# Kernel tuning notes

Measured on AMD Instinct MI355X. Metric: run time of the kernel, lower is better.

The kernel has to match this reference:

```python
import jax, jax.numpy as jnp
import numpy as np

B, S, D = 4, 2048, 768
H = 12
HD = D // H  # 64


def setup_inputs() -> dict:
    key = jax.random.key(0)
    k1, k2, k3 = jax.random.split(key, 3)
    scale_qkv = (6.0 / (D + 3 * D)) ** 0.5  # xavier_uniform bound
    scale_o = (6.0 / (D + D)) ** 0.5
    return {
        "x": jax.random.normal(k1, (B, S, D), dtype=jnp.float32),
        "w_qkv": jax.random.uniform(k2, (3 * D, D), dtype=jnp.float32, minval=-scale_qkv, maxval=scale_qkv),
        "b_qkv": jnp.zeros((3 * D,), dtype=jnp.float32),
        "w_o": jax.random.uniform(k3, (D, D), dtype=jnp.float32, minval=-scale_o, maxval=scale_o),
        "b_o": jnp.zeros((D,), dtype=jnp.float32),
    }


def reference(x, w_qkv, b_qkv, w_o, b_o):
    b, s, _ = x.shape
    # qkv projection: [B,S,3D]
    qkv = jnp.einsum("bsd,ed->bse", x, w_qkv) + b_qkv
    # [B,S,H,3*HD] -> [B,H,S,3*HD]
    qkv = qkv.reshape(b, s, H, 3 * HD).transpose(0, 2, 1, 3)
    q, k, v = jnp.split(qkv, 3, axis=-1)  # each [B,H,S,HD]
    # scaled dot-product attention (full score matrix, as in source)
    attn_logits = jnp.einsum("bhqd,bhkd->bhqk", q, k) / np.sqrt(HD).astype(np.float32)
    attention = jax.nn.softmax(attn_logits, axis=-1)
    values = jnp.einsum("bhqk,bhkd->bhqd", attention, v)
    # merge heads: [B,S,D]
    values = values.transpose(0, 2, 1, 3).reshape(b, s, D)
    out = jnp.einsum("bsd,ed->bse", values, w_o) + b_o
    return out
```

## Files before the change

kernel.cpp:

```cpp
#include <hip/hip_runtime.h>
#include <hip/hip_bf16.h>

#define BB 4
#define SS 2048
#define DD 768
#define HH 12
#define HDD 64
#define QKVW 2304

typedef _Float16 h8 __attribute__((ext_vector_type(8)));
typedef _Float16 h2 __attribute__((ext_vector_type(2)));
typedef __fp16 fp16x2 __attribute__((ext_vector_type(2)));
typedef float f4 __attribute__((ext_vector_type(4)));
typedef unsigned int u4 __attribute__((ext_vector_type(4)));

struct __align__(8) Half4 { _Float16 x, y, z, w; };
struct __align__(8) H2x2 { h2 a, b; };

#define QSCALE 0.18033688011112042f

__device__ __forceinline__ h2 pk_cvt(float a, float b) {
    fp16x2 r = __builtin_amdgcn_cvt_pkrtz(a, b);
    return __builtin_bit_cast(h2, r);
}

__device__ __forceinline__ float fexp2(float x) {
    return __builtin_amdgcn_exp2f(x);
}

__device__ __forceinline__ void pl_swap32(unsigned &a, unsigned &b) {
    asm("v_permlane32_swap_b32 %0, %1" : "+v"(a), "+v"(b));
}
__device__ __forceinline__ void pl_swap16(unsigned &a, unsigned &b) {
    asm("v_permlane16_swap_b32 %0, %1" : "+v"(a), "+v"(b));
}

#define N4_X   (BB * SS * DD / 4)
#define N4_WQ  (QKVW * DD / 4)
#define N4_WO  (DD * DD / 4)
#define N4_ALL (N4_X + N4_WQ + N4_WO)

__global__ __launch_bounds__(256) void cvt_all(const float* __restrict__ x,
                                               const float* __restrict__ wq,
                                               const float* __restrict__ wo,
                                               _Float16* __restrict__ xh,
                                               _Float16* __restrict__ wqh,
                                               _Float16* __restrict__ woh) {
    int i = blockIdx.x * 256 + threadIdx.x;
    const float* src;
    _Float16* dst;
    if (i < N4_X) {
        src = x; dst = xh;
    } else if (i < N4_X + N4_WQ) {
        i -= N4_X; src = wq; dst = wqh;
    } else {
        i -= N4_X + N4_WQ; src = wo; dst = woh;
    }
    const float4 v = ((const float4*)src)[i];
    Half4 h = {(_Float16)v.x, (_Float16)v.y, (_Float16)v.z, (_Float16)v.w};
    ((Half4*)dst)[i] = h;
}

__device__ __forceinline__ void gload16(const _Float16* g, _Float16* l) {
    __builtin_amdgcn_global_load_lds(
        (const __attribute__((address_space(1))) unsigned int*)g,
        (__attribute__((address_space(3))) unsigned int*)l, 16, 0, 0);
}

template <int EPI>
__global__ __launch_bounds__(256) void gemm_f16(const _Float16* __restrict__ A,
                                                const _Float16* __restrict__ B,
                                                const float* __restrict__ bias,
                                                float* __restrict__ Cf,
                                                _Float16* __restrict__ Ch,
                                                _Float16* __restrict__ VTg,
                                                int M, int N, int K) {
    __shared__ alignas(16) _Float16 Ash[128 * 64];
    __shared__ alignas(16) _Float16 Bsh[128 * 64];

    const int tid = threadIdx.x;
    const int lane = tid & 63;
    const int w = tid >> 6;
    const int l15 = lane & 15;
    const int qd = lane >> 4;
    const int wm = w & 1;
    const int wn = w >> 1;
    const int m0 = blockIdx.y * 128;
    const int n0 = blockIdx.x * 128;
    const int ldsb = w * 512;

    f4 acc[4][4];
#pragma unroll
    for (int mt = 0; mt < 4; ++mt)
#pragma unroll
        for (int nt = 0; nt < 4; ++nt) acc[mt][nt] = (f4){0.f, 0.f, 0.f, 0.f};

    const _Float16* Ab = A + (size_t)m0 * K;
    const _Float16* Bb = B + (size_t)n0 * K;

    const int srow = tid >> 3;
    const int cg = ((tid & 7) ^ (srow & 7)) * 8;
    const int x7 = l15 & 7;

    for (int k0 = 0; k0 < K; k0 += 64) {
        __syncthreads();
#pragma unroll
        for (int i = 0; i < 4; ++i) {
            const size_t gsrc = (size_t)(i * 32 + srow) * K + k0 + cg;
            gload16(Ab + gsrc, Ash + i * 2048 + ldsb);
            gload16(Bb + gsrc, Bsh + i * 2048 + ldsb);
        }
        __syncthreads();

#pragma unroll
        for (int s = 0; s < 2; ++s) {
            h8 aF[4], bF[4];
#pragma unroll
            for (int mt = 0; mt < 4; ++mt)
                aF[mt] = *(const h8*)&Ash[(wm * 64 + mt * 16 + l15) * 64
                                          + (((s * 4 + qd) ^ x7) << 3)];
#pragma unroll
            for (int nt = 0; nt < 4; ++nt)
                bF[nt] = *(const h8*)&Bsh[(wn * 64 + nt * 16 + l15) * 64
                                          + (((s * 4 + qd) ^ x7) << 3)];
#pragma unroll
            for (int mt = 0; mt < 4; ++mt)
#pragma unroll
                for (int nt = 0; nt < 4; ++nt)
                    acc[mt][nt] = __builtin_amdgcn_mfma_f32_16x16x32_f16(
                        bF[nt], aF[mt], acc[mt][nt], 0, 0, 0);
        }
    }

#pragma unroll
    for (int mt = 0; mt < 4; ++mt) {
        const int m = m0 + wm * 64 + mt * 16 + l15;
#pragma unroll
        for (int nt = 0; nt < 4; ++nt) {
            const int nb = n0 + wn * 64 + nt * 16 + qd * 4;
            const float4 bv = *(const float4*)(bias + nb);
            f4 v = acc[mt][nt];
            v[0] += bv.x; v[1] += bv.y; v[2] += bv.z; v[3] += bv.w;
            if (EPI == 0) {
                *(float4*)(Cf + (size_t)m * N + nb) = (float4){v[0], v[1], v[2], v[3]};
            } else {
                const int typ = (nb >> 6) % 3;
                if (typ == 2) {
                    const int h_ = nb / 192;
                    const int d0 = nb - h_ * 192 - 128;
                    _Float16* vtp = VTg + ((size_t)(m >> 11) * 768 + h_ * 64 + d0) * 2048
                                    + (m & 2047);
                    vtp[0] = (_Float16)v[0];
                    vtp[2048] = (_Float16)v[1];
                    vtp[2 * 2048] = (_Float16)v[2];
                    vtp[3 * 2048] = (_Float16)v[3];
                } else {
                    if (typ == 0) {
                        v[0] *= QSCALE; v[1] *= QSCALE; v[2] *= QSCALE; v[3] *= QSCALE;
                    }
                    H2x2 pk;
                    pk.a = pk_cvt(v[0], v[1]);
                    pk.b = pk_cvt(v[2], v[3]);
                    *(H2x2*)(Ch + (size_t)m * N + nb) = pk;
                }
            }
        }
    }
}

__global__ __launch_bounds__(256, 3) void attn_mfma(const _Float16* __restrict__ qkvh,
                                                    const _Float16* __restrict__ vT,
                                                    _Float16* __restrict__ vh) {
    __shared__ alignas(16) _Float16 Kh[2][64 * 64];
    __shared__ alignas(16) _Float16 VTs[2][64 * 64];

    const int tid = threadIdx.x;
    const int lane = tid & 63;
    const int w = tid >> 6;
    const int l15 = lane & 15;
    const int qd = lane >> 4;
    const int h = blockIdx.y;
    const int b = blockIdx.z;
    const int qbase = blockIdx.x * 128 + w * 32;

    const size_t bhrow = (size_t)b * SS;
    const int hcol = h * 192;
    const int x7 = l15 & 7;

    h8 bQ[2][2];
#pragma unroll
    for (int nt = 0; nt < 2; ++nt)
#pragma unroll
        for (int kc = 0; kc < 2; ++kc)
            bQ[nt][kc] = *(const h8*)(qkvh + (bhrow + qbase + nt * 16 + l15) * QKVW
                                      + hcol + kc * 32 + qd * 8);

    f4 O[4][2];
#pragma unroll
    for (int dt = 0; dt < 4; ++dt)
#pragma unroll
        for (int nt = 0; nt < 2; ++nt) O[dt][nt] = (f4){0.f, 0.f, 0.f, 0.f};
    f4 lacc[2] = {(f4){0.f, 0.f, 0.f, 0.f}, (f4){0.f, 0.f, 0.f, 0.f}};

    h8 ones;
#pragma unroll
    for (int i = 0; i < 8; ++i) ones[i] = (_Float16)1.0f;

    const int srow = tid >> 3;
    const int cgx = ((tid & 7) ^ (srow & 7)) << 3;
    const _Float16* kgbase = qkvh + bhrow * QKVW + hcol + 64 + cgx;
    const _Float16* vgbase = vT + ((size_t)b * 768 + h * 64) * 2048 + cgx;
    const int ldso = w * 512;

    auto stage = [&](int kt, int buf) {
#pragma unroll
        for (int i = 0; i < 2; ++i) {
            gload16(kgbase + (size_t)(kt * 64 + i * 32 + srow) * QKVW,
                    &Kh[buf][i * 2048 + ldso]);
            gload16(vgbase + (size_t)(i * 32 + srow) * 2048 + kt * 64,
                    &VTs[buf][i * 2048 + ldso]);
        }
    };

    stage(0, 0);

    for (int kt = 0; kt < SS / 64; ++kt) {
        const int buf = kt & 1;
        __syncthreads();
        if (kt + 1 < SS / 64) stage(kt + 1, buf ^ 1);

        h8 aK[4][2];
#pragma unroll
        for (int mt = 0; mt < 4; ++mt)
#pragma unroll
            for (int kc = 0; kc < 2; ++kc)
                aK[mt][kc] = *(const h8*)&Kh[buf][(mt * 16 + l15) * 64
                                                  + (((kc * 4 + qd) ^ x7) << 3)];
        h8 aV[4][2];
#pragma unroll
        for (int dt = 0; dt < 4; ++dt)
#pragma unroll
            for (int kc = 0; kc < 2; ++kc)
                aV[dt][kc] = *(const h8*)&VTs[buf][(dt * 16 + l15) * 64
                                                   + (((kc * 4 + qd) ^ x7) << 3)];

        h8 bP[2][2];
#pragma unroll
        for (int nt = 0; nt < 2; ++nt) {
            unsigned c[4][2];
            __builtin_amdgcn_s_setprio(1);
#pragma unroll
            for (int mt = 0; mt < 4; ++mt) {
                f4 z = (f4){0.f, 0.f, 0.f, 0.f};
                z = __builtin_amdgcn_mfma_f32_16x16x32_f16(aK[mt][0], bQ[nt][0], z, 0, 0, 0);
                z = __builtin_amdgcn_mfma_f32_16x16x32_f16(aK[mt][1], bQ[nt][1], z, 0, 0, 0);
                c[mt][0] = __builtin_bit_cast(unsigned, pk_cvt(fexp2(z[0]), fexp2(z[1])));
                c[mt][1] = __builtin_bit_cast(unsigned, pk_cvt(fexp2(z[2]), fexp2(z[3])));
            }
            __builtin_amdgcn_s_setprio(0);
#pragma unroll
            for (int kc = 0; kc < 2; ++kc) {
                unsigned x0 = c[2 * kc][0], y0 = c[2 * kc + 1][0];
                pl_swap32(x0, y0);
                pl_swap16(x0, y0);
                unsigned x1 = c[2 * kc][1], y1 = c[2 * kc + 1][1];
                pl_swap32(x1, y1);
                pl_swap16(x1, y1);
                u4 t = (u4){x0, x1, y0, y1};
                bP[nt][kc] = __builtin_bit_cast(h8, t);
            }
        }

        __builtin_amdgcn_s_setprio(1);
#pragma unroll
        for (int nt = 0; nt < 2; ++nt) {
            lacc[nt] = __builtin_amdgcn_mfma_f32_16x16x32_f16(ones, bP[nt][0], lacc[nt], 0, 0, 0);
            lacc[nt] = __builtin_amdgcn_mfma_f32_16x16x32_f16(ones, bP[nt][1], lacc[nt], 0, 0, 0);
        }
#pragma unroll
        for (int dt = 0; dt < 4; ++dt)
#pragma unroll
            for (int nt = 0; nt < 2; ++nt) {
                O[dt][nt] = __builtin_amdgcn_mfma_f32_16x16x32_f16(aV[dt][0], bP[nt][0], O[dt][nt], 0, 0, 0);
                O[dt][nt] = __builtin_amdgcn_mfma_f32_16x16x32_f16(aV[dt][1], bP[nt][1], O[dt][nt], 0, 0, 0);
            }
        __builtin_amdgcn_s_setprio(0);
    }

#pragma unroll
    for (int nt = 0; nt < 2; ++nt) {
        const float linv = 1.0f / lacc[nt][0];
        const size_t row = bhrow + qbase + nt * 16 + l15;
#pragma unroll
        for (int dt = 0; dt < 4; ++dt) {
            f4 o = O[dt][nt];
            Half4 oh;
            oh.x = (_Float16)(o[0] * linv);
            oh.y = (_Float16)(o[1] * linv);
            oh.z = (_Float16)(o[2] * linv);
            oh.w = (_Float16)(o[3] * linv);
            *(Half4*)(vh + row * DD + h * 64 + dt * 16 + qd * 4) = oh;
        }
    }
}

extern "C" void kernel_launch(void* const* d_in, const int* in_sizes, int n_in,
                              void* d_out, int out_size, void* d_ws, size_t ws_size,
                              hipStream_t stream) {
    const float* x     = (const float*)d_in[0];
    const float* w_qkv = (const float*)d_in[1];
    const float* b_qkv = (const float*)d_in[2];
    const float* w_o   = (const float*)d_in[3];
    const float* b_o   = (const float*)d_in[4];
    float* out = (float*)d_out;

    const int M = BB * SS;

    _Float16* p = (_Float16*)d_ws;
    _Float16* qkv_h = p;  p += (size_t)M * QKVW;
    _Float16* vT = p;     p += (size_t)BB * DD * SS;
    _Float16* xh = p;     p += (size_t)M * DD;
    _Float16* vh = p;     p += (size_t)M * DD;
    _Float16* wqh = p;    p += (size_t)QKVW * DD;
    _Float16* woh = p;    p += (size_t)DD * DD;

    cvt_all<<<N4_ALL / 256, 256, 0, stream>>>(x, w_qkv, w_o, xh, wqh, woh);

    gemm_f16<1><<<dim3(QKVW / 128, M / 128), 256, 0, stream>>>(
        xh, wqh, b_qkv, nullptr, qkv_h, vT, M, QKVW, DD);

    attn_mfma<<<dim3(SS / 128, HH, BB), 256, 0, stream>>>(qkv_h, vT, vh);

    gemm_f16<0><<<dim3(DD / 128, M / 128), 256, 0, stream>>>(
        vh, woh, b_o, out, nullptr, nullptr, M, DD, DD);
}
```

Baseline: 221.6 us.

## Split attention key tiles across two wave groups with LDS reduction

Doubles the attention block to 512 threads so each 64-key tile is split between two wave groups, each handling 32 keys for the same 32 query rows. Partial O accumulators and row sums are combined through shared memory at the end before normalization. This halves per-wave MFMA and LDS work per tile, aiming at more latency hiding and wave-level parallelism. The cost is extra redundant Q loads and exp work per wave, plus an epilogue with several barriers and LDS traffic. Softmax has no max subtraction, so a plain sum of partials is correct.

```diff
diff --git a/kernel.cpp b/kernel.cpp
--- a/kernel.cpp
+++ b/kernel.cpp
@@ -168,7 +168,7 @@
     }
 }
 
-__global__ __launch_bounds__(256, 3) void attn_mfma(const _Float16* __restrict__ qkvh,
+__global__ __launch_bounds__(512, 6) void attn_mfma(const _Float16* __restrict__ qkvh,
                                                     const _Float16* __restrict__ vT,
                                                     _Float16* __restrict__ vh) {
     __shared__ alignas(16) _Float16 Kh[2][64 * 64];
@@ -177,11 +177,13 @@
     const int tid = threadIdx.x;
     const int lane = tid & 63;
     const int w = tid >> 6;
+    const int qg = w & 3;
+    const int kh = w >> 2;
     const int l15 = lane & 15;
     const int qd = lane >> 4;
     const int h = blockIdx.y;
     const int b = blockIdx.z;
-    const int qbase = blockIdx.x * 128 + w * 32;
+    const int qbase = blockIdx.x * 128 + qg * 32;
 
     const size_t bhrow = (size_t)b * SS;
     const int hcol = h * 192;
@@ -206,20 +208,15 @@
 #pragma unroll
     for (int i = 0; i < 8; ++i) ones[i] = (_Float16)1.0f;
 
-    const int srow = tid >> 3;
-    const int cgx = ((tid & 7) ^ (srow & 7)) << 3;
-    const _Float16* kgbase = qkvh + bhrow * QKVW + hcol + 64 + cgx;
-    const _Float16* vgbase = vT + ((size_t)b * 768 + h * 64) * 2048 + cgx;
+    const int trow = (tid >> 3) & 63;
+    const int cgx = ((tid & 7) ^ (trow & 7)) << 3;
+    const _Float16* kgbase = qkvh + (bhrow + trow) * QKVW + hcol + 64 + cgx;
+    const _Float16* vgbase = vT + ((size_t)b * 768 + h * 64 + trow) * 2048 + cgx;
     const int ldso = w * 512;
 
     auto stage = [&](int kt, int buf) {
-#pragma unroll
-        for (int i = 0; i < 2; ++i) {
-            gload16(kgbase + (size_t)(kt * 64 + i * 32 + srow) * QKVW,
-                    &Kh[buf][i * 2048 + ldso]);
-            gload16(vgbase + (size_t)(i * 32 + srow) * 2048 + kt * 64,
-                    &VTs[buf][i * 2048 + ldso]);
-        }
+        gload16(kgbase + (size_t)kt * 64 * QKVW, &Kh[buf][ldso]);
+        gload16(vgbase + kt * 64, &VTs[buf][ldso]);
     };
 
     stage(0, 0);
@@ -229,28 +226,26 @@
         __syncthreads();
         if (kt + 1 < SS / 64) stage(kt + 1, buf ^ 1);
 
-        h8 aK[4][2];
-#pragma unroll
-        for (int mt = 0; mt < 4; ++mt)
+        h8 aK[2][2];
+#pragma unroll
+        for (int mt = 0; mt < 2; ++mt)
 #pragma unroll
             for (int kc = 0; kc < 2; ++kc)
-                aK[mt][kc] = *(const h8*)&Kh[buf][(mt * 16 + l15) * 64
+                aK[mt][kc] = *(const h8*)&Kh[buf][(kh * 32 + mt * 16 + l15) * 64
                                                   + (((kc * 4 + qd) ^ x7) << 3)];
-        h8 aV[4][2];
+        h8 aV[4];
 #pragma unroll
         for (int dt = 0; dt < 4; ++dt)
-#pragma unroll
-            for (int kc = 0; kc < 2; ++kc)
-                aV[dt][kc] = *(const h8*)&VTs[buf][(dt * 16 + l15) * 64
-                                                   + (((kc * 4 + qd) ^ x7) << 3)];
-
-        h8 bP[2][2];
+            aV[dt] = *(const h8*)&VTs[buf][(dt * 16 + l15) * 64
+                                           + (((kh * 4 + qd) ^ x7) << 3)];
+
+        h8 bP[2];
 #pragma unroll
         for (int nt = 0; nt < 2; ++nt) {
-            unsigned c[4][2];
+            unsigned c[2][2];
             __builtin_amdgcn_s_setprio(1);
 #pragma unroll
-            for (int mt = 0; mt < 4; ++mt) {
+            for (int mt = 0; mt < 2; ++mt) {
                 f4 z = (f4){0.f, 0.f, 0.f, 0.f};
                 z = __builtin_amdgcn_mfma_f32_16x16x32_f16(aK[mt][0], bQ[nt][0], z, 0, 0, 0);
                 z = __builtin_amdgcn_mfma_f32_16x16x32_f16(aK[mt][1], bQ[nt][1], z, 0, 0, 0);
@@ -258,48 +253,77 @@
                 c[mt][1] = __builtin_bit_cast(unsigned, pk_cvt(fexp2(z[2]), fexp2(z[3])));
             }
             __builtin_amdgcn_s_setprio(0);
-#pragma unroll
-            for (int kc = 0; kc < 2; ++kc) {
-                unsigned x0 = c[2 * kc][0], y0 = c[2 * kc + 1][0];
-                pl_swap32(x0, y0);
-                pl_swap16(x0, y0);
-                unsigned x1 = c[2 * kc][1], y1 = c[2 * kc + 1][1];
-                pl_swap32(x1, y1);
-                pl_swap16(x1, y1);
-                u4 t = (u4){x0, x1, y0, y1};
-                bP[nt][kc] = __builtin_bit_cast(h8, t);
+            unsigned x0 = c[0][0], y0 = c[1][0];
+            pl_swap32(x0, y0);
+            pl_swap16(x0, y0);
+            unsigned x1 = c[0][1], y1 = c[1][1];
+            pl_swap32(x1, y1);
+            pl_swap16(x1, y1);
+            u4 t = (u4){x0, x1, y0, y1};
+            bP[nt] = __builtin_bit_cast(h8, t);
+        }
+
+        __builtin_amdgcn_s_setprio(1);
+#pragma unroll
+        for (int nt = 0; nt < 2; ++nt)
+            lacc[nt] = __builtin_amdgcn_mfma_f32_16x16x32_f16(ones, bP[nt], lacc[nt], 0, 0, 0);
+#pragma unroll
+        for (int dt = 0; dt < 4; ++dt)
+#pragma unroll
+            for (int nt = 0; nt < 2; ++nt)
+                O[dt][nt] = __builtin_amdgcn_mfma_f32_16x16x32_f16(aV[dt], bP[nt], O[dt][nt], 0, 0, 0);
+        __builtin_amdgcn_s_setprio(0);
+    }
+
+    __syncthreads();
+    f4* cmb = (f4*)&Kh[0][0];
+    float* lcmb = (float*)&VTs[0][0];
+    const int ps = (qg * 64 + lane) * 4;
+
+    if (kh == 1) {
+#pragma unroll
+        for (int r = 0; r < 2; ++r)
+#pragma unroll
+            for (int nt = 0; nt < 2; ++nt) cmb[ps + r * 2 + nt] = O[r][nt];
+    }
+    __syncthreads();
+    if (kh == 0) {
+#pragma unroll
+        for (int r = 0; r < 2; ++r)
+#pragma unroll
+            for (int nt = 0; nt < 2; ++nt) O[r][nt] += cmb[ps + r * 2 + nt];
+    }
+    __syncthreads();
+    if (kh == 1) {
+#pragma unroll
+        for (int r = 2; r < 4; ++r)
+#pragma unroll
+            for (int nt = 0; nt < 2; ++nt) cmb[ps + (r - 2) * 2 + nt] = O[r][nt];
+        lcmb[(qg * 64 + lane) * 2 + 0] = lacc[0][0];
+        lcmb[(qg * 64 + lane) * 2 + 1] = lacc[1][0];
+    }
+    __syncthreads();
+    if (kh == 0) {
+#pragma unroll
+        for (int r = 2; r < 4; ++r)
+#pragma unroll
+            for (int nt = 0; nt < 2; ++nt) O[r][nt] += cmb[ps + (r - 2) * 2 + nt];
+
+#pragma unroll
+        for (int nt = 0; nt < 2; ++nt) {
+            const float lt = lacc[nt][0] + lcmb[(qg * 64 + lane) * 2 + nt];
+            const float linv = 1.0f / lt;
+            const size_t row = bhrow + qbase + nt * 16 + l15;
+#pragma unroll
+            for (int dt = 0; dt < 4; ++dt) {
+                f4 o = O[dt][nt];
+                Half4 oh;
+                oh.x = (_Float16)(o[0] * linv);
+                oh.y = (_Float16)(o[1] * linv);
+                oh.z = (_Float16)(o[2] * linv);
+                oh.w = (_Float16)(o[3] * linv);
+                *(Half4*)(vh + row * DD + h * 64 + dt * 16 + qd * 4) = oh;
             }
-        }
-
-        __builtin_amdgcn_s_setprio(1);
-#pragma unroll
-        for (int nt = 0; nt < 2; ++nt) {
-            lacc[nt] = __builtin_amdgcn_mfma_f32_16x16x32_f16(ones, bP[nt][0], lacc[nt], 0, 0, 0);
-            lacc[nt] = __builtin_amdgcn_mfma_f32_16x16x32_f16(ones, bP[nt][1], lacc[nt], 0, 0, 0);
-        }
-#pragma unroll
-        for (int dt = 0; dt < 4; ++dt)
-#pragma unroll
-            for (int nt = 0; nt < 2; ++nt) {
-                O[dt][nt] = __builtin_amdgcn_mfma_f32_16x16x32_f16(aV[dt][0], bP[nt][0], O[dt][nt], 0, 0, 0);
-                O[dt][nt] = __builtin_amdgcn_mfma_f32_16x16x32_f16(aV[dt][1], bP[nt][1], O[dt][nt], 0, 0, 0);
-            }
-        __builtin_amdgcn_s_setprio(0);
-    }
-
-#pragma unroll
-    for (int nt = 0; nt < 2; ++nt) {
-        const float linv = 1.0f / lacc[nt][0];
-        const size_t row = bhrow + qbase + nt * 16 + l15;
-#pragma unroll
-        for (int dt = 0; dt < 4; ++dt) {
-            f4 o = O[dt][nt];
-            Half4 oh;
-            oh.x = (_Float16)(o[0] * linv);
-            oh.y = (_Float16)(o[1] * linv);
-            oh.z = (_Float16)(o[2] * linv);
-            oh.w = (_Float16)(o[3] * linv);
-            *(Half4*)(vh + row * DD + h * 64 + dt * 16 + qd * 4) = oh;
         }
     }
 }
@@ -329,7 +353,7 @@
     gemm_f16<1><<<dim3(QKVW / 128, M / 128), 256, 0, stream>>>(
         xh, wqh, b_qkv, nullptr, qkv_h, vT, M, QKVW, DD);
 
-    attn_mfma<<<dim3(SS / 128, HH, BB), 256, 0, stream>>>(qkv_h, vT, vh);
+    attn_mfma<<<dim3(SS / 128, HH, BB), 512, 0, stream>>>(qkv_h, vT, vh);
 
     gemm_f16<0><<<dim3(DD / 128, M / 128), 256, 0, stream>>>(
         vh, woh, b_o, out, nullptr, nullptr, M, DD, DD);
```

Result: slower. 516.6 us (+133.1%).
